# Optimization experiments

Measured on AMD Instinct MI355X. Metric: run time of the kernel, lower is better.

Reference implementation:

```python
import jax, jax.numpy as jnp
import numpy as np

HIDDEN = 1024
NUM_HEADS = 16
HEAD_DIM = HIDDEN // NUM_HEADS
GRID_SIZE = 5
SPLINE_ORDER = 3
NUM_COEF = GRID_SIZE + SPLINE_ORDER  # 8


def make_grid(in_features):
    # efficient-kan default grid: range [-1, 1], extended by spline_order on each side
    h = 2.0 / GRID_SIZE
    g = jnp.arange(-SPLINE_ORDER, GRID_SIZE + SPLINE_ORDER + 1, dtype=jnp.float32) * h - 1.0
    return jnp.broadcast_to(g, (in_features, g.shape[0]))  # (in, G+2k+1)


def b_splines(x, grid):
    # x: (N, in); grid: (in, G+2k+1) -> bases (N, in, G+k)
    x = x[..., None]
    bases = ((x >= grid[:, :-1]) & (x < grid[:, 1:])).astype(x.dtype)
    for k in range(1, SPLINE_ORDER + 1):
        left = (x - grid[:, : -(k + 1)]) / (grid[:, k:-1] - grid[:, : -(k + 1)])
        right = (grid[:, k + 1 :] - x) / (grid[:, k + 1 :] - grid[:, 1:-k])
        bases = left * bases[..., :-1] + right * bases[..., 1:]
    return bases


def kan_linear(x, base_w, spline_w, spline_scaler):
    # x: (..., in); base_w: (out, in); spline_w: (out, in, C); spline_scaler: (out, in)
    in_f = x.shape[-1]
    x2 = x.reshape(-1, in_f)
    base = jax.nn.silu(x2) @ base_w.T
    bases = b_splines(x2, make_grid(in_f))                      # (N, in, C)
    sw = spline_w * spline_scaler[..., None]                    # (out, in, C)
    spline = bases.reshape(x2.shape[0], -1) @ sw.reshape(sw.shape[0], -1).T
    return (base + spline).reshape(*x.shape[:-1], base_w.shape[0])


def apply_rope(x):
    # x: (B, H, S, D); interleaved rotary (lucidrains convention), theta=10000
    d, s = x.shape[-1], x.shape[-2]
    inv_freq = 1.0 / (10000.0 ** (jnp.arange(0, d, 2, dtype=jnp.float32) / d))
    freqs = jnp.arange(s, dtype=jnp.float32)[:, None] * inv_freq[None, :]  # (S, d/2)
    cos = jnp.repeat(jnp.cos(freqs), 2, axis=-1)
    sin = jnp.repeat(jnp.sin(freqs), 2, axis=-1)
    x1, x2 = x[..., 0::2], x[..., 1::2]
    rot = jnp.stack((-x2, x1), axis=-1).reshape(x.shape)
    return x * cos + rot * sin


def setup_inputs() -> dict:
    key = jax.random.key(0)
    ks = jax.random.split(key, 10)
    B, S, H = 2, 2048, HIDDEN
    H3 = 3 * H
    scale = 0.02
    return {
        "q": jax.random.normal(ks[0], (B, S, H), jnp.float32),
        "k": jax.random.normal(ks[1], (B, S, H), jnp.float32),
        "v": jax.random.normal(ks[2], (B, S, H), jnp.float32),
        "attn_mask": jnp.zeros((S, S), jnp.float32),
        "qkv_base_w": jax.random.normal(ks[3], (H3, H3), jnp.float32) * scale,
        "qkv_spline_w": jax.random.normal(ks[4], (H3, H3, NUM_COEF), jnp.float32) * scale,
        "qkv_scaler": jnp.ones((H3, H3), jnp.float32),
        "out_base_w": jax.random.normal(ks[5], (H, H), jnp.float32) * scale,
        "out_spline_w": jax.random.normal(ks[6], (H, H, NUM_COEF), jnp.float32) * scale,
        "out_scaler": jnp.ones((H, H), jnp.float32),
    }


def reference(q, k, v, attn_mask, qkv_base_w, qkv_spline_w, qkv_scaler,
              out_base_w, out_spline_w, out_scaler):
    B, S, H = q.shape
    x = jnp.concatenate((q, k, v), axis=2)                       # (B, S, 3H)
    qkv = kan_linear(x, qkv_base_w, qkv_spline_w, qkv_scaler)    # (B, S, 3H)
    qkv = qkv.reshape(B, S, NUM_HEADS, 3 * HEAD_DIM).transpose(0, 2, 1, 3)
    queries, keys, values = jnp.split(qkv, 3, axis=-1)           # each (B, nh, S, hd)
    queries = apply_rope(queries)
    keys = apply_rope(keys)
    scores = jnp.einsum("bhqd,bhkd->bhqk", queries, keys) / (HEAD_DIM ** 0.5) + attn_mask
    attention = jax.nn.softmax(scores, axis=-1)
    context = jnp.einsum("bhqk,bhkd->bhqd", attention, values)
    context = context.transpose(0, 2, 1, 3).reshape(B, S, H)
    return kan_linear(context, out_base_w, out_spline_w, out_scaler)
```

## Files before the change

### kernel.cpp

```cpp
#include <hip/hip_runtime.h>
#include <hip/hip_bf16.h>
#include <stdint.h>

typedef __bf16 bf16;
typedef __attribute__((ext_vector_type(8))) __bf16 bf16x8;
typedef __attribute__((ext_vector_type(4))) float f32x4;

#define DEVI __device__ __forceinline__

constexpr int BATCH = 2, SEQ = 2048, HID = 1024, NHEAD = 16, HDIM = 64;
constexpr int H3 = 3072;
constexpr int MROWS = BATCH * SEQ;
constexpr int KEXP = 9;
constexpr int K1DIM = H3 * KEXP;
constexpr int K2DIM = HID * KEXP;

constexpr size_t WQ_OFF  = 0;
constexpr size_t AQ_OFF  = 169869312;
constexpr size_t CQ_OFF  = AQ_OFF + 226492416;
constexpr size_t QR_OFF  = CQ_OFF + 50331648;
constexpr size_t KR_OFF  = QR_OFF + 8388608;
constexpr size_t VB_OFF  = KR_OFF + 8388608;
constexpr size_t CTX_OFF = VB_OFF + 8388608;
constexpr size_t A2_OFF  = 0;
constexpr size_t W2_OFF  = 75497472;

DEVI void gld_lds16(const void* g, void* l) {
  __builtin_amdgcn_global_load_lds((const __attribute__((address_space(1))) void*)g,
                                   (__attribute__((address_space(3))) void*)l, 16, 0, 0);
}

DEVI void silu_bases(float x, float* o9) {
  o9[0] = x / (1.0f + __expf(-x));
  float g[12];
#pragma unroll
  for (int j = 0; j < 12; ++j) g[j] = (float)(j - 3) * 0.4f - 1.0f;
  float b[11];
#pragma unroll
  for (int j = 0; j < 11; ++j) b[j] = (x >= g[j] && x < g[j + 1]) ? 1.0f : 0.0f;
#pragma unroll
  for (int k = 1; k <= 3; ++k) {
    const float inv = (k == 1) ? 2.5f : (k == 2) ? 1.25f : (1.0f / 1.2f);
#pragma unroll
    for (int j = 0; j + k < 11; ++j) {
      b[j] = (x - g[j]) * inv * b[j] + (g[j + k + 1] - x) * inv * b[j + 1];
    }
  }
#pragma unroll
  for (int c = 0; c < 8; ++c) o9[1 + c] = b[c];
}

__global__ __launch_bounds__(256)
void wprep_kernel(const float* __restrict__ bw, const float* __restrict__ sw,
                  const float* __restrict__ sc, bf16* __restrict__ W, int KK) {
  __shared__ bf16 buf[256 * KEXP];
  const int tid = threadIdx.x;
  const int n = blockIdx.y;
  const int i0 = blockIdx.x * 256;
  const size_t idx = (size_t)n * KK + i0 + tid;
  float base = bw[idx];
  float scal = sc[idx];
  const float4* sp = (const float4*)(sw + idx * 8);
  float4 s0 = sp[0], s1 = sp[1];
  bf16* o = buf + tid * KEXP;
  o[0] = (bf16)base;
  o[1] = (bf16)(s0.x * scal); o[2] = (bf16)(s0.y * scal);
  o[3] = (bf16)(s0.z * scal); o[4] = (bf16)(s0.w * scal);
  o[5] = (bf16)(s1.x * scal); o[6] = (bf16)(s1.y * scal);
  o[7] = (bf16)(s1.z * scal); o[8] = (bf16)(s1.w * scal);
  __syncthreads();
  bf16* dst = W + (size_t)n * KK * KEXP + (size_t)i0 * KEXP;
#pragma unroll
  for (int j = tid; j < 256 * KEXP / 8; j += 256)
    *(bf16x8*)(dst + j * 8) = *(const bf16x8*)(buf + j * 8);
}

__global__ __launch_bounds__(256)
void act_qkv_kernel(const float* __restrict__ qin, const float* __restrict__ kin,
                    const float* __restrict__ vin, bf16* __restrict__ A) {
  __shared__ bf16 buf[256 * KEXP];
  const int tid = threadIdx.x;
  const int m = blockIdx.y;
  const int i0 = blockIdx.x * 256;
  const int i = i0 + tid;
  const int which = i >> 10, off = i & 1023;
  const float* src = (which == 0) ? qin : (which == 1) ? kin : vin;
  float x = src[(size_t)m * HID + off];
  float o9[9];
  silu_bases(x, o9);
  bf16* o = buf + tid * KEXP;
#pragma unroll
  for (int c = 0; c < 9; ++c) o[c] = (bf16)o9[c];
  __syncthreads();
  bf16* dst = A + (size_t)m * K1DIM + (size_t)i0 * KEXP;
#pragma unroll
  for (int j = tid; j < 256 * KEXP / 8; j += 256)
    *(bf16x8*)(dst + j * 8) = *(const bf16x8*)(buf + j * 8);
}

__global__ __launch_bounds__(256)
void act_out_kernel(const float* __restrict__ ctx, bf16* __restrict__ A) {
  __shared__ bf16 buf[256 * KEXP];
  const int tid = threadIdx.x;
  const int m = blockIdx.y;
  const int i0 = blockIdx.x * 256;
  float x = ctx[(size_t)m * HID + i0 + tid];
  float o9[9];
  silu_bases(x, o9);
  bf16* o = buf + tid * KEXP;
#pragma unroll
  for (int c = 0; c < 9; ++c) o[c] = (bf16)o9[c];
  __syncthreads();
  bf16* dst = A + (size_t)m * K2DIM + (size_t)i0 * KEXP;
#pragma unroll
  for (int j = tid; j < 256 * KEXP / 8; j += 256)
    *(bf16x8*)(dst + j * 8) = *(const bf16x8*)(buf + j * 8);
}

__global__ __launch_bounds__(256, 2)
void gemm_kernel(const bf16* __restrict__ A, const bf16* __restrict__ Bw,
                 float* __restrict__ C, int N, int K) {
  __shared__ bf16 As[128 * 64];
  __shared__ bf16 Bs[128 * 64];
  const int tid = threadIdx.x;
  const int lane = tid & 63;
  const int l15 = lane & 15, lq = lane >> 4;
  const int wid = tid >> 6;
  const int wm = (wid >> 1) * 64, wn = (wid & 1) * 64;
  const int bm = blockIdx.y, bn = blockIdx.x;
  f32x4 acc[4][4] = {};
  const int srow = tid >> 3;
  const int schk = (tid & 7) ^ (srow & 7);
  const bf16* aB = A + (size_t)(bm * 128 + srow) * K + schk * 8;
  const bf16* bB = Bw + (size_t)(bn * 128 + srow) * K + schk * 8;

  int aoff[2][4], boff[2][4];
#pragma unroll
  for (int ks = 0; ks < 2; ++ks) {
#pragma unroll
    for (int f = 0; f < 4; ++f) {
      int arow = wm + f * 16 + l15;
      int brow = wn + f * 16 + l15;
      aoff[ks][f] = arow * 64 + (((ks * 4 + lq) ^ (arow & 7)) * 8);
      boff[ks][f] = brow * 64 + (((ks * 4 + lq) ^ (brow & 7)) * 8);
    }
  }

  for (int kt = 0; kt < K; kt += 64) {
#pragma unroll
    for (int r = 0; r < 4; ++r) {
      gld_lds16(aB + (size_t)(r * 32) * K + kt, As + r * 2048 + tid * 8);
      gld_lds16(bB + (size_t)(r * 32) * K + kt, Bs + r * 2048 + tid * 8);
    }
    __syncthreads();
#pragma unroll
    for (int ks = 0; ks < 2; ++ks) {
      bf16x8 af[4], bfr[4];
#pragma unroll
      for (int mf = 0; mf < 4; ++mf)
        af[mf] = *(const bf16x8*)&As[aoff[ks][mf]];
#pragma unroll
      for (int nf = 0; nf < 4; ++nf)
        bfr[nf] = *(const bf16x8*)&Bs[boff[ks][nf]];
#pragma unroll
      for (int mf = 0; mf < 4; ++mf)
#pragma unroll
        for (int nf = 0; nf < 4; ++nf)
          acc[mf][nf] = __builtin_amdgcn_mfma_f32_16x16x32_bf16(af[mf], bfr[nf], acc[mf][nf], 0, 0, 0);
    }
    __syncthreads();
  }
#pragma unroll
  for (int mf = 0; mf < 4; ++mf)
#pragma unroll
    for (int nf = 0; nf < 4; ++nf)
#pragma unroll
      for (int r = 0; r < 4; ++r) {
        int row = bm * 128 + wm + mf * 16 + lq * 4 + r;
        int col = bn * 128 + wn + nf * 16 + l15;
        C[(size_t)row * N + col] = acc[mf][nf][r];
      }
}

__global__ void rope_kernel(const float* __restrict__ Cq, bf16* __restrict__ qr,
                            bf16* __restrict__ kr, bf16* __restrict__ vb) {
  int idx = blockIdx.x * blockDim.x + threadIdx.x;
  int p = idx & 31;
  int h = (idx >> 5) & 15;
  int m = idx >> 9;
  int s = m & (SEQ - 1);
  int b = m >> 11;
  const float* row = Cq + (size_t)m * H3 + h * 192;
  float q0 = row[2 * p], q1 = row[2 * p + 1];
  float k0 = row[64 + 2 * p], k1 = row[64 + 2 * p + 1];
  float v0 = row[128 + 2 * p], v1 = row[128 + 2 * p + 1];
  float invf = expf(-(float)p * (9.210340371976184f / 32.0f));
  float fr = (float)s * invf;
  float sn, cs;
  sincosf(fr, &sn, &cs);
  size_t o = (((size_t)(b * NHEAD + h)) * SEQ + s) * 64 + 2 * p;
  qr[o] = (bf16)(q0 * cs - q1 * sn); qr[o + 1] = (bf16)(q1 * cs + q0 * sn);
  kr[o] = (bf16)(k0 * cs - k1 * sn); kr[o + 1] = (bf16)(k1 * cs + k0 * sn);
  vb[o] = (bf16)v0; vb[o + 1] = (bf16)v1;
}

__global__ __launch_bounds__(256, 2)
void attn_kernel(const bf16* __restrict__ qr, const bf16* __restrict__ kr,
                 const bf16* __restrict__ vb, const float* __restrict__ mask,
                 float* __restrict__ ctx) {
  __shared__ bf16 Kt[64 * 64];
  __shared__ bf16 Vt[64 * 64];
  __shared__ bf16 Pl[4][16 * 64];
  const int tid = threadIdx.x, lane = tid & 63, wid = tid >> 6;
  const int l15 = lane & 15, lq = lane >> 4;
  const int qt = blockIdx.x, bh = blockIdx.y;
  const int b = bh >> 4, hh = bh & 15;
  const size_t baseQ = ((size_t)bh * SEQ + qt * 64 + wid * 16) * 64;
  bf16x8 aq[2];
  aq[0] = *(const bf16x8*)&qr[baseQ + (size_t)l15 * 64 + 0 + lq * 8];
  aq[1] = *(const bf16x8*)&qr[baseQ + (size_t)l15 * 64 + 32 + lq * 8];
  float mrow[4], lrow[4];
  f32x4 oacc[4] = {};
#pragma unroll
  for (int r = 0; r < 4; ++r) { mrow[r] = -1e30f; lrow[r] = 0.0f; }
  const float scale = 0.125f;
  const int krow = tid >> 3;
  const int kchk = (tid & 7) ^ (krow & 7);
  for (int kv0 = 0; kv0 < SEQ; kv0 += 64) {
    const bf16* kBase = kr + ((size_t)bh * SEQ + kv0 + krow) * 64 + kchk * 8;
#pragma unroll
    for (int r = 0; r < 2; ++r)
      gld_lds16(kBase + (size_t)(r * 32) * 64, Kt + r * 2048 + tid * 8);
#pragma unroll
    for (int r = 0; r < 2; ++r) {
      int row = r * 32 + (tid >> 3);
      int c8 = (tid & 7) * 8;
      bf16x8 vv = *(const bf16x8*)&vb[((size_t)bh * SEQ + kv0 + row) * 64 + c8];
#pragma unroll
      for (int e = 0; e < 8; ++e) {
        int d = c8 + e;
        Vt[d * 64 + (((row >> 3) ^ (d & 7)) << 3) + (row & 7)] = vv[e];
      }
    }
    __syncthreads();
    f32x4 sacc[4] = {};
#pragma unroll
    for (int k0 = 0; k0 < 2; ++k0) {
#pragma unroll
      for (int nf = 0; nf < 4; ++nf) {
        bf16x8 bk = *(const bf16x8*)&Kt[(nf * 16 + l15) * 64 + (((k0 * 4 + lq) ^ (l15 & 7)) << 3)];
        sacc[nf] = __builtin_amdgcn_mfma_f32_16x16x32_bf16(aq[k0], bk, sacc[nf], 0, 0, 0);
      }
    }
    const int qg0 = qt * 64 + wid * 16 + lq * 4;
#pragma unroll
    for (int nf = 0; nf < 4; ++nf) {
      int kvg = kv0 + nf * 16 + l15;
#pragma unroll
      for (int r = 0; r < 4; ++r)
        sacc[nf][r] = sacc[nf][r] * scale + mask[(size_t)(qg0 + r) * SEQ + kvg];
    }
    float fac[4];
#pragma unroll
    for (int r = 0; r < 4; ++r) {
      float v = fmaxf(fmaxf(sacc[0][r], sacc[1][r]), fmaxf(sacc[2][r], sacc[3][r]));
      v = fmaxf(v, __shfl_xor(v, 1));
      v = fmaxf(v, __shfl_xor(v, 2));
      v = fmaxf(v, __shfl_xor(v, 4));
      v = fmaxf(v, __shfl_xor(v, 8));
      float mnew = fmaxf(mrow[r], v);
      fac[r] = __expf(mrow[r] - mnew);
      mrow[r] = mnew;
    }
    float rs[4] = {0, 0, 0, 0};
#pragma unroll
    for (int nf = 0; nf < 4; ++nf)
#pragma unroll
      for (int r = 0; r < 4; ++r) {
        float pv = __expf(sacc[nf][r] - mrow[r]);
        sacc[nf][r] = pv;
        rs[r] += pv;
      }
#pragma unroll
    for (int r = 0; r < 4; ++r) {
      float v = rs[r];
      v += __shfl_xor(v, 1); v += __shfl_xor(v, 2);
      v += __shfl_xor(v, 4); v += __shfl_xor(v, 8);
      lrow[r] = lrow[r] * fac[r] + v;
    }
#pragma unroll
    for (int nf = 0; nf < 4; ++nf)
#pragma unroll
      for (int r = 0; r < 4; ++r) {
        int qrow = lq * 4 + r;
        int col = nf * 16 + l15;
        Pl[wid][qrow * 64 + ((((col >> 3) ^ (qrow & 7))) << 3) + (col & 7)] = (bf16)sacc[nf][r];
      }
#pragma unroll
    for (int nf = 0; nf < 4; ++nf)
#pragma unroll
      for (int r = 0; r < 4; ++r)
        oacc[nf][r] *= fac[r];
#pragma unroll
    for (int k0 = 0; k0 < 2; ++k0) {
      bf16x8 ap = *(const bf16x8*)&Pl[wid][l15 * 64 + (((k0 * 4 + lq) ^ (l15 & 7)) << 3)];
#pragma unroll
      for (int nf = 0; nf < 4; ++nf) {
        bf16x8 bv = *(const bf16x8*)&Vt[(nf * 16 + l15) * 64 + (((k0 * 4 + lq) ^ (l15 & 7)) << 3)];
        oacc[nf] = __builtin_amdgcn_mfma_f32_16x16x32_bf16(ap, bv, oacc[nf], 0, 0, 0);
      }
    }
    __syncthreads();
  }
#pragma unroll
  for (int nf = 0; nf < 4; ++nf)
#pragma unroll
    for (int r = 0; r < 4; ++r) {
      int row = qt * 64 + wid * 16 + lq * 4 + r;
      int col = hh * 64 + nf * 16 + l15;
      ctx[((size_t)b * SEQ + row) * HID + col] = oacc[nf][r] / lrow[r];
    }
}

extern "C" void kernel_launch(void* const* d_in, const int* in_sizes, int n_in,
                              void* d_out, int out_size, void* d_ws, size_t ws_size,
                              hipStream_t stream) {
  const float* qin    = (const float*)d_in[0];
  const float* kin    = (const float*)d_in[1];
  const float* vin    = (const float*)d_in[2];
  const float* mask   = (const float*)d_in[3];
  const float* qkv_bw = (const float*)d_in[4];
  const float* qkv_sw = (const float*)d_in[5];
  const float* qkv_sc = (const float*)d_in[6];
  const float* out_bw = (const float*)d_in[7];
  const float* out_sw = (const float*)d_in[8];
  const float* out_sc = (const float*)d_in[9];
  char* ws = (char*)d_ws;
  bf16* Wq  = (bf16*)(ws + WQ_OFF);
  bf16* Aq  = (bf16*)(ws + AQ_OFF);
  float* Cq = (float*)(ws + CQ_OFF);
  bf16* qr  = (bf16*)(ws + QR_OFF);
  bf16* kr  = (bf16*)(ws + KR_OFF);
  bf16* vb  = (bf16*)(ws + VB_OFF);
  float* ctx = (float*)(ws + CTX_OFF);
  bf16* A2  = (bf16*)(ws + A2_OFF);
  bf16* W2  = (bf16*)(ws + W2_OFF);

  wprep_kernel<<<dim3(H3 / 256, H3), 256, 0, stream>>>(qkv_bw, qkv_sw, qkv_sc, Wq, H3);
  act_qkv_kernel<<<dim3(H3 / 256, MROWS), 256, 0, stream>>>(qin, kin, vin, Aq);
  gemm_kernel<<<dim3(H3 / 128, MROWS / 128), 256, 0, stream>>>(Aq, Wq, Cq, H3, K1DIM);
  rope_kernel<<<(MROWS * NHEAD * 32) / 256, 256, 0, stream>>>(Cq, qr, kr, vb);
  attn_kernel<<<dim3(SEQ / 64, BATCH * NHEAD), 256, 0, stream>>>(qr, kr, vb, mask, ctx);
  act_out_kernel<<<dim3(HID / 256, MROWS), 256, 0, stream>>>(ctx, A2);
  wprep_kernel<<<dim3(HID / 256, HID), 256, 0, stream>>>(out_bw, out_sw, out_sc, W2, HID);
  gemm_kernel<<<dim3(HID / 128, MROWS / 128), 256, 0, stream>>>(A2, W2, (float*)d_out, HID, K2DIM);
}
```

Before: 1.196 ms.

## Triple-buffer GEMM LDS tiles with K=32 stages and vmcnt-based waits

Rewrites the bf16 MFMA GEMM main loop into a three-stage software pipeline. It uses 32-wide K tiles in triple-buffered LDS, prefetches two stages ahead with global_load_lds, and waits with s_waitcnt vmcnt plus a single barrier per iteration instead of two __syncthreads. It also raises the launch-bounds occupancy hint to 3 blocks per CU, adjusts the LDS swizzle for the narrower rows, and raises wave priority around the MFMA block. The goal is to hide global-load latency behind matrix math, at the cost of smaller per-stage work, tighter register limits, and reliance on manual waitcnt correctness.

```diff
diff --git a/kernel.cpp b/kernel.cpp
--- a/kernel.cpp
+++ b/kernel.cpp
@@ -29,6 +29,10 @@
   __builtin_amdgcn_global_load_lds((const __attribute__((address_space(1))) void*)g,
                                    (__attribute__((address_space(3))) void*)l, 16, 0, 0);
 }
+
+#define WAITVM(n) asm volatile("s_waitcnt vmcnt(" #n ")" ::: "memory")
+#define MEMFENCE() asm volatile("" ::: "memory")
+#define BARRIER() do { __builtin_amdgcn_s_barrier(); asm volatile("" ::: "memory"); } while (0)
 
 DEVI void silu_bases(float x, float* o9) {
   o9[0] = x / (1.0f + __expf(-x));
@@ -117,11 +121,11 @@
     *(bf16x8*)(dst + j * 8) = *(const bf16x8*)(buf + j * 8);
 }
 
-__global__ __launch_bounds__(256, 2)
+__global__ __launch_bounds__(256, 3)
 void gemm_kernel(const bf16* __restrict__ A, const bf16* __restrict__ Bw,
                  float* __restrict__ C, int N, int K) {
-  __shared__ bf16 As[128 * 64];
-  __shared__ bf16 Bs[128 * 64];
+  __shared__ bf16 As[3][128 * 32];
+  __shared__ bf16 Bs[3][128 * 32];
   const int tid = threadIdx.x;
   const int lane = tid & 63;
   const int l15 = lane & 15, lq = lane >> 4;
@@ -129,47 +133,62 @@
   const int wm = (wid >> 1) * 64, wn = (wid & 1) * 64;
   const int bm = blockIdx.y, bn = blockIdx.x;
   f32x4 acc[4][4] = {};
-  const int srow = tid >> 3;
-  const int schk = (tid & 7) ^ (srow & 7);
+  const int srow = tid >> 2;
+  const int schk = (tid & 3) ^ ((srow >> 1) & 3);
   const bf16* aB = A + (size_t)(bm * 128 + srow) * K + schk * 8;
   const bf16* bB = Bw + (size_t)(bn * 128 + srow) * K + schk * 8;
 
-  int aoff[2][4], boff[2][4];
-#pragma unroll
-  for (int ks = 0; ks < 2; ++ks) {
-#pragma unroll
-    for (int f = 0; f < 4; ++f) {
-      int arow = wm + f * 16 + l15;
-      int brow = wn + f * 16 + l15;
-      aoff[ks][f] = arow * 64 + (((ks * 4 + lq) ^ (arow & 7)) * 8);
-      boff[ks][f] = brow * 64 + (((ks * 4 + lq) ^ (brow & 7)) * 8);
-    }
+  int aoff[4], boff[4];
+#pragma unroll
+  for (int f = 0; f < 4; ++f) {
+    int arow = wm + f * 16 + l15;
+    int brow = wn + f * 16 + l15;
+    aoff[f] = arow * 32 + ((lq ^ ((arow >> 1) & 3)) * 8);
+    boff[f] = brow * 32 + ((lq ^ ((brow >> 1) & 3)) * 8);
   }
 
-  for (int kt = 0; kt < K; kt += 64) {
-#pragma unroll
-    for (int r = 0; r < 4; ++r) {
-      gld_lds16(aB + (size_t)(r * 32) * K + kt, As + r * 2048 + tid * 8);
-      gld_lds16(bB + (size_t)(r * 32) * K + kt, Bs + r * 2048 + tid * 8);
-    }
-    __syncthreads();
-#pragma unroll
-    for (int ks = 0; ks < 2; ++ks) {
-      bf16x8 af[4], bfr[4];
-#pragma unroll
-      for (int mf = 0; mf < 4; ++mf)
-        af[mf] = *(const bf16x8*)&As[aoff[ks][mf]];
+#define GSTAGE(bi_, kt_)                                                        \
+  do {                                                                          \
+    bf16* dA_ = &As[bi_][0];                                                    \
+    bf16* dB_ = &Bs[bi_][0];                                                    \
+    gld_lds16(aB + (kt_), dA_ + tid * 8);                                       \
+    gld_lds16(aB + (size_t)64 * K + (kt_), dA_ + 2048 + tid * 8);               \
+    gld_lds16(bB + (kt_), dB_ + tid * 8);                                       \
+    gld_lds16(bB + (size_t)64 * K + (kt_), dB_ + 2048 + tid * 8);               \
+  } while (0)
+
+  const int nt = K >> 5;
+  GSTAGE(0, 0);
+  MEMFENCE();
+  GSTAGE(1, (size_t)32);
+  WAITVM(0);
+  BARRIER();
+  for (int t = 0; t < nt; ++t) {
+    if (t + 2 < nt) { GSTAGE((t + 2) % 3, (size_t)(t + 2) * 32); MEMFENCE(); }
+    const bf16* as = &As[t % 3][0];
+    const bf16* bs = &Bs[t % 3][0];
+    bf16x8 af[4], bfr[4];
+#pragma unroll
+    for (int mf = 0; mf < 4; ++mf) af[mf] = *(const bf16x8*)(as + aoff[mf]);
+#pragma unroll
+    for (int nf = 0; nf < 4; ++nf) bfr[nf] = *(const bf16x8*)(bs + boff[nf]);
+    __builtin_amdgcn_s_setprio(1);
+#pragma unroll
+    for (int mf = 0; mf < 4; ++mf)
 #pragma unroll
       for (int nf = 0; nf < 4; ++nf)
-        bfr[nf] = *(const bf16x8*)&Bs[boff[ks][nf]];
-#pragma unroll
-      for (int mf = 0; mf < 4; ++mf)
-#pragma unroll
-        for (int nf = 0; nf < 4; ++nf)
-          acc[mf][nf] = __builtin_amdgcn_mfma_f32_16x16x32_bf16(af[mf], bfr[nf], acc[mf][nf], 0, 0, 0);
-    }
-    __syncthreads();
+        acc[mf][nf] = __builtin_amdgcn_mfma_f32_16x16x32_bf16(af[mf], bfr[nf], acc[mf][nf], 0, 0, 0);
+    __builtin_amdgcn_s_setprio(0);
+    if (t < nt - 2) {
+      WAITVM(4);
+      BARRIER();
+    } else if (t == nt - 2) {
+      WAITVM(0);
+      BARRIER();
+    }
   }
+#undef GSTAGE
+
 #pragma unroll
   for (int mf = 0; mf < 4; ++mf)
 #pragma unroll
```

Measured after the change: 1.334 ms. 1.12x slower.

## Double-buffer attention K/V tiles and write V pre-transposed from RoPE kernel

Applied to the files above, without the earlier changes.

The RoPE kernel now writes V transposed (head dim by sequence), so the attention kernel can stream V straight into LDS with async global-to-LDS loads instead of a per-element transposing scatter. K and V tiles are double-buffered so the next tile loads while the current one is computed, with explicit vmcnt waits and barriers. The 1/sqrt(d) softmax scale is folded into Q during RoPE. The trade-offs are more LDS per block and strided, uncoalesced 2-byte stores for V in the RoPE kernel. Attention is only one of several kernels in the pipeline, which caps how much the total can change.

```diff
diff --git a/kernel.cpp b/kernel.cpp
--- a/kernel.cpp
+++ b/kernel.cpp
@@ -29,6 +29,10 @@
   __builtin_amdgcn_global_load_lds((const __attribute__((address_space(1))) void*)g,
                                    (__attribute__((address_space(3))) void*)l, 16, 0, 0);
 }
+
+#define WAITVM0() asm volatile("s_waitcnt vmcnt(0)" ::: "memory")
+#define MEMFENCE() asm volatile("" ::: "memory")
+#define BARRIER() do { __builtin_amdgcn_s_barrier(); asm volatile("" ::: "memory"); } while (0)
 
 DEVI void silu_bases(float x, float* o9) {
   o9[0] = x / (1.0f + __expf(-x));
@@ -183,7 +187,7 @@
 }
 
 __global__ void rope_kernel(const float* __restrict__ Cq, bf16* __restrict__ qr,
-                            bf16* __restrict__ kr, bf16* __restrict__ vb) {
+                            bf16* __restrict__ kr, bf16* __restrict__ vt) {
   int idx = blockIdx.x * blockDim.x + threadIdx.x;
   int p = idx & 31;
   int h = (idx >> 5) & 15;
@@ -198,18 +202,21 @@
   float fr = (float)s * invf;
   float sn, cs;
   sincosf(fr, &sn, &cs);
-  size_t o = (((size_t)(b * NHEAD + h)) * SEQ + s) * 64 + 2 * p;
-  qr[o] = (bf16)(q0 * cs - q1 * sn); qr[o + 1] = (bf16)(q1 * cs + q0 * sn);
+  const int bh = b * NHEAD + h;
+  size_t o = ((size_t)bh * SEQ + s) * 64 + 2 * p;
+  qr[o] = (bf16)((q0 * cs - q1 * sn) * 0.125f);
+  qr[o + 1] = (bf16)((q1 * cs + q0 * sn) * 0.125f);
   kr[o] = (bf16)(k0 * cs - k1 * sn); kr[o + 1] = (bf16)(k1 * cs + k0 * sn);
-  vb[o] = (bf16)v0; vb[o + 1] = (bf16)v1;
+  vt[((size_t)bh * 64 + 2 * p) * SEQ + s] = (bf16)v0;
+  vt[((size_t)bh * 64 + 2 * p + 1) * SEQ + s] = (bf16)v1;
 }
 
 __global__ __launch_bounds__(256, 2)
 void attn_kernel(const bf16* __restrict__ qr, const bf16* __restrict__ kr,
-                 const bf16* __restrict__ vb, const float* __restrict__ mask,
+                 const bf16* __restrict__ vt, const float* __restrict__ mask,
                  float* __restrict__ ctx) {
-  __shared__ bf16 Kt[64 * 64];
-  __shared__ bf16 Vt[64 * 64];
+  __shared__ bf16 Kt[2][64 * 64];
+  __shared__ bf16 Vt[2][64 * 64];
   __shared__ bf16 Pl[4][16 * 64];
   const int tid = threadIdx.x, lane = tid & 63, wid = tid >> 6;
   const int l15 = lane & 15, lq = lane >> 4;
@@ -223,32 +230,33 @@
   f32x4 oacc[4] = {};
 #pragma unroll
   for (int r = 0; r < 4; ++r) { mrow[r] = -1e30f; lrow[r] = 0.0f; }
-  const float scale = 0.125f;
-  const int krow = tid >> 3;
-  const int kchk = (tid & 7) ^ (krow & 7);
+  const int srow = tid >> 3;
+  const int schk = (tid & 7) ^ (srow & 7);
+  const bf16* kBase = kr + ((size_t)bh * SEQ + srow) * 64 + schk * 8;
+  const bf16* vBase = vt + ((size_t)bh * 64 + srow) * SEQ + schk * 8;
+
+#define ASTAGE(bi_, kv_)                                                        \
+  do {                                                                          \
+    gld_lds16(kBase + (size_t)(kv_) * 64, &Kt[bi_][0] + tid * 8);               \
+    gld_lds16(kBase + (size_t)((kv_) + 32) * 64, &Kt[bi_][0] + 2048 + tid * 8); \
+    gld_lds16(vBase + (kv_), &Vt[bi_][0] + tid * 8);                            \
+    gld_lds16(vBase + (size_t)32 * SEQ + (kv_), &Vt[bi_][0] + 2048 + tid * 8);  \
+  } while (0)
+
+  ASTAGE(0, 0);
+  WAITVM0();
+  BARRIER();
   for (int kv0 = 0; kv0 < SEQ; kv0 += 64) {
-    const bf16* kBase = kr + ((size_t)bh * SEQ + kv0 + krow) * 64 + kchk * 8;
-#pragma unroll
-    for (int r = 0; r < 2; ++r)
-      gld_lds16(kBase + (size_t)(r * 32) * 64, Kt + r * 2048 + tid * 8);
-#pragma unroll
-    for (int r = 0; r < 2; ++r) {
-      int row = r * 32 + (tid >> 3);
-      int c8 = (tid & 7) * 8;
-      bf16x8 vv = *(const bf16x8*)&vb[((size_t)bh * SEQ + kv0 + row) * 64 + c8];
-#pragma unroll
-      for (int e = 0; e < 8; ++e) {
-        int d = c8 + e;
-        Vt[d * 64 + (((row >> 3) ^ (d & 7)) << 3) + (row & 7)] = vv[e];
-      }
-    }
-    __syncthreads();
+    const int cur = (kv0 >> 6) & 1;
+    if (kv0 + 64 < SEQ) { ASTAGE(cur ^ 1, kv0 + 64); MEMFENCE(); }
+    const bf16* kt = &Kt[cur][0];
+    const bf16* vtl = &Vt[cur][0];
     f32x4 sacc[4] = {};
 #pragma unroll
     for (int k0 = 0; k0 < 2; ++k0) {
 #pragma unroll
       for (int nf = 0; nf < 4; ++nf) {
-        bf16x8 bk = *(const bf16x8*)&Kt[(nf * 16 + l15) * 64 + (((k0 * 4 + lq) ^ (l15 & 7)) << 3)];
+        bf16x8 bk = *(const bf16x8*)&kt[(nf * 16 + l15) * 64 + (((k0 * 4 + lq) ^ (l15 & 7)) << 3)];
         sacc[nf] = __builtin_amdgcn_mfma_f32_16x16x32_bf16(aq[k0], bk, sacc[nf], 0, 0, 0);
       }
     }
@@ -258,7 +266,7 @@
       int kvg = kv0 + nf * 16 + l15;
 #pragma unroll
       for (int r = 0; r < 4; ++r)
-        sacc[nf][r] = sacc[nf][r] * scale + mask[(size_t)(qg0 + r) * SEQ + kvg];
+        sacc[nf][r] += mask[(size_t)(qg0 + r) * SEQ + kvg];
     }
     float fac[4];
 #pragma unroll
@@ -306,12 +314,14 @@
       bf16x8 ap = *(const bf16x8*)&Pl[wid][l15 * 64 + (((k0 * 4 + lq) ^ (l15 & 7)) << 3)];
 #pragma unroll
       for (int nf = 0; nf < 4; ++nf) {
-        bf16x8 bv = *(const bf16x8*)&Vt[(nf * 16 + l15) * 64 + (((k0 * 4 + lq) ^ (l15 & 7)) << 3)];
+        bf16x8 bv = *(const bf16x8*)&vtl[(nf * 16 + l15) * 64 + (((k0 * 4 + lq) ^ (l15 & 7)) << 3)];
         oacc[nf] = __builtin_amdgcn_mfma_f32_16x16x32_bf16(ap, bv, oacc[nf], 0, 0, 0);
       }
     }
-    __syncthreads();
+    WAITVM0();
+    BARRIER();
   }
+#undef ASTAGE
 #pragma unroll
   for (int nf = 0; nf < 4; ++nf)
 #pragma unroll
@@ -341,7 +351,7 @@
   float* Cq = (float*)(ws + CQ_OFF);
   bf16* qr  = (bf16*)(ws + QR_OFF);
   bf16* kr  = (bf16*)(ws + KR_OFF);
-  bf16* vb  = (bf16*)(ws + VB_OFF);
+  bf16* vt  = (bf16*)(ws + VB_OFF);
   float* ctx = (float*)(ws + CTX_OFF);
   bf16* A2  = (bf16*)(ws + A2_OFF);
   bf16* W2  = (bf16*)(ws + W2_OFF);
@@ -349,8 +359,8 @@
   wprep_kernel<<<dim3(H3 / 256, H3), 256, 0, stream>>>(qkv_bw, qkv_sw, qkv_sc, Wq, H3);
   act_qkv_kernel<<<dim3(H3 / 256, MROWS), 256, 0, stream>>>(qin, kin, vin, Aq);
   gemm_kernel<<<dim3(H3 / 128, MROWS / 128), 256, 0, stream>>>(Aq, Wq, Cq, H3, K1DIM);
-  rope_kernel<<<(MROWS * NHEAD * 32) / 256, 256, 0, stream>>>(Cq, qr, kr, vb);
-  attn_kernel<<<dim3(SEQ / 64, BATCH * NHEAD), 256, 0, stream>>>(qr, kr, vb, mask, ctx);
+  rope_kernel<<<(MROWS * NHEAD * 32) / 256, 256, 0, stream>>>(Cq, qr, kr, vt);
+  attn_kernel<<<dim3(SEQ / 64, BATCH * NHEAD), 256, 0, stream>>>(qr, kr, vt, mask, ctx);
   act_out_kernel<<<dim3(HID / 256, MROWS), 256, 0, stream>>>(ctx, A2);
   wprep_kernel<<<dim3(HID / 256, HID), 256, 0, stream>>>(out_bw, out_sw, out_sc, W2, HID);
   gemm_kernel<<<dim3(HID / 128, MROWS / 128), 256, 0, stream>>>(A2, W2, (float*)d_out, HID, K2DIM);
```

New measurement: 1.151 ms. 1.04x faster.
